# Optimization experiments

Hardware: AMD Instinct MI355X
Metric: run time of the kernel (lower is better)

Reference implementation:

```python
import jax, jax.numpy as jnp
import numpy as np

B, T, F, H = 256, 128, 128, 512

def setup_inputs() -> dict:
    key = jax.random.key(0)
    ks = jax.random.split(key, 20)
    def xavier(k, shape):
        fan_in, fan_out = shape[1], shape[0]
        lim = np.sqrt(6.0 / (fan_in + fan_out)).astype(np.float32)
        return jax.random.uniform(k, shape, jnp.float32, -lim, lim)
    inp = {
        "x": jax.random.normal(ks[0], (B, T, F), jnp.float32),
        "m": (jax.random.uniform(ks[1], (B, T, F)) < 0.8).astype(jnp.float32),
        "d": jax.random.uniform(ks[2], (B, T, F), jnp.float32),
        "target_x": jax.random.normal(ks[3], (B, T, F), jnp.float32),
        "target_mask": (jax.random.uniform(ks[4], (B, T, F)) < 0.2).astype(jnp.float32),
        # TemporalDecay h: W [H,F], b [H]
        "td_h_W": xavier(ks[5], (H, F)), "td_h_b": jnp.zeros((H,), jnp.float32),
        # TemporalDecay x (diag): W [F,F], b [F]
        "td_x_W": xavier(ks[6], (F, F)), "td_x_b": jnp.zeros((F,), jnp.float32),
        # hist_reg Linear(H->F)
        "hist_W": xavier(ks[7], (F, H)), "hist_b": jnp.zeros((F,), jnp.float32),
        "feat_W": xavier(ks[8], (F, F)), "feat_b": jnp.zeros((F,), jnp.float32),
        # weight_combine Linear(2F->F)
        "wc_W": xavier(ks[9], (F, 2 * F)), "wc_b": jnp.zeros((F,), jnp.float32),
        # LSTMCell(2F -> H), PyTorch gate order i,f,g,o
        "W_ih": xavier(ks[10], (4 * H, 2 * F)), "W_hh": xavier(ks[11], (4 * H, H)),
        "b_ih": jnp.zeros((4 * H,), jnp.float32), "b_hh": jnp.zeros((4 * H,), jnp.float32),
    }
    return inp

def _rits_forward(x, m, d, target_x, target_mask,
                  td_h_W, td_h_b, td_x_W, td_x_b,
                  hist_W, hist_b, feat_W, feat_b, wc_W, wc_b,
                  W_ih, W_hh, b_ih, b_hh):
    Bx, Tx, Fx = x.shape
    Hx = td_h_W.shape[0]
    feat_mask = (1.0 - jnp.eye(Fx, dtype=x.dtype))
    feat_Wm_T = (feat_W * feat_mask).T              # [F,F]
    td_x_diag = jnp.diagonal(td_x_W)                # diag mask reduces matmul to elementwise

    def step(carry, inp):
        h, c, loss = carry
        x_t, m_t, d_t, tgt_t, ev_t = inp
        gamma_h = jnp.exp(-jax.nn.relu(d_t @ td_h_W.T + td_h_b))    # [B,H]
        gamma_x = jnp.exp(-jax.nn.relu(d_t * td_x_diag + td_x_b))   # [B,F]
        h = h * gamma_h
        x_hist = h @ hist_W.T + hist_b                              # [B,F]
        x_c = m_t * x_t + (1.0 - m_t) * x_hist
        z_h = x_c @ feat_Wm_T + feat_b
        alpha = jax.nn.sigmoid(jnp.concatenate([gamma_x, m_t], axis=1) @ wc_W.T + wc_b)
        c_h = alpha * z_h + (1.0 - alpha) * x_hist
        c_c = m_t * x_t + (1.0 - m_t) * c_h
        inputs = jnp.concatenate([c_c, m_t], axis=1)                # [B,2F]
        gates = inputs @ W_ih.T + b_ih + h @ W_hh.T + b_hh          # [B,4H]
        i_g, f_g, g_g, o_g = jnp.split(gates, 4, axis=1)
        c = jax.nn.sigmoid(f_g) * c + jax.nn.sigmoid(i_g) * jnp.tanh(g_g)
        h = jax.nn.sigmoid(o_g) * jnp.tanh(c)
        denom = ev_t.sum() + 1e-8
        loss = loss + (((x_hist - tgt_t) ** 2 * ev_t).sum()
                       + ((z_h - tgt_t) ** 2 * ev_t).sum()
                       + ((c_h - tgt_t) ** 2 * ev_t).sum()) / denom
        return (h, c, loss), c_c

    h0 = jnp.zeros((Bx, Hx), x.dtype)
    c0 = jnp.zeros((Bx, Hx), x.dtype)
    tm = lambda a: jnp.swapaxes(a, 0, 1)  # time-major [T,B,F]
    (_, _, loss), imps = jax.lax.scan(
        step, (h0, c0, jnp.float32(0.0)),
        (tm(x), tm(m), tm(d), tm(target_x), tm(target_mask)))
    imputations = jnp.swapaxes(imps, 0, 1)  # [B,T,F]
    return imputations, loss / max(Tx, 1)

def reference(x, m, d, target_x, target_mask,
              td_h_W, td_h_b, td_x_W, td_x_b,
              hist_W, hist_b, feat_W, feat_b, wc_W, wc_b,
              W_ih, W_hh, b_ih, b_hh):
    return _rits_forward(x, m, d, target_x, target_mask,
                         td_h_W, td_h_b, td_x_W, td_x_b,
                         hist_W, hist_b, feat_W, feat_b, wc_W, wc_b,
                         W_ih, W_hh, b_ih, b_hh)
```

## Files before the change

kernel.cpp:

```cpp
#include <hip/hip_runtime.h>

#define DEVINL __device__ __forceinline__

namespace {
constexpr int B = 256, T = 128, F = 128, H = 512;
constexpr int NBLK = 256;
constexpr int NTHR = 1024;

constexpr size_t OFF_NUM    = 0;
constexpr size_t OFF_DEN    = 128;
constexpr size_t OFF_WQCC   = 256;
constexpr size_t OFF_WQH    = OFF_WQCC + 64 * 2048;
constexpr size_t OFF_FSCC   = OFF_WQH + 128 * 2048;
constexpr size_t OFF_FSCHG  = OFF_FSCC + 2048;
constexpr size_t OFF_HISTQ  = OFF_FSCHG + 2048;
constexpr size_t OFF_FSCH   = OFF_HISTQ + 128 * 128;
constexpr size_t OFF_TD2    = OFF_FSCH + 128;
constexpr size_t OFF_FEAT2  = OFF_TD2 + 64 * 512;
constexpr size_t OFF_WC2    = OFF_FEAT2 + 64 * 128;
constexpr size_t OFF_BSUM   = OFF_WC2 + 128 * 128;
constexpr size_t OFF_FDIAG  = OFF_BSUM + 2048;
constexpr size_t WS_WORDS   = OFF_FDIAG + 128;

constexpr float ACT_S  = 15.875f;
constexpr float DEQ_CC = 1.f / (127.f * 15.875f);
constexpr float DEQ_H  = 1.f / (127.f * 127.f);
}

typedef _Float16 h2_t __attribute__((ext_vector_type(2)));

DEVINL h2_t as_h2(unsigned u) { union { unsigned u; h2_t h; } c; c.u = u; return c.h; }
DEVINL unsigned pack2(float a, float b) {
  union { h2_t h; unsigned u; } c;
  c.h = h2_t{(_Float16)a, (_Float16)b};
  return c.u;
}

#if defined(__has_builtin)
#if __has_builtin(__builtin_amdgcn_fdot2)
#define HAVE_FDOT2 1
#endif
#if __has_builtin(__builtin_amdgcn_sdot4)
#define HAVE_SDOT4 1
#endif
#endif
#ifdef HAVE_FDOT2
DEVINL float fdot2(h2_t a, h2_t b, float c) { return __builtin_amdgcn_fdot2(a, b, c, false); }
#else
DEVINL float fdot2(h2_t a, h2_t b, float c) {
  return fmaf((float)a.x, (float)b.x, fmaf((float)a.y, (float)b.y, c));
}
#endif
#ifdef HAVE_SDOT4
DEVINL int sdot4(int a, int b, int c) { return __builtin_amdgcn_sdot4(a, b, c, false); }
#else
DEVINL int sdot4(int a, int b, int c) {
  return c + ((a << 24) >> 24) * ((b << 24) >> 24)
           + ((a << 16) >> 24) * ((b << 16) >> 24)
           + ((a << 8) >> 24) * ((b << 8) >> 24)
           + (a >> 24) * (b >> 24);
}
#endif

DEVINL float fast_sig(float x)  { return 1.f / (1.f + __expf(-x)); }
DEVINL float fast_tanh(float x) { return 1.f - 2.f / (1.f + __expf(2.f * x)); }

DEVINL float wave_sum(float v) {
#pragma unroll
  for (int s = 32; s; s >>= 1) v += __shfl_down(v, s, 64);
  return v;
}
DEVINL float wave_max(float v) {
#pragma unroll
  for (int s = 32; s; s >>= 1) v = fmaxf(v, __shfl_down(v, s, 64));
  return v;
}

__global__ void prep_f16(const float* __restrict__ td_h_W, const float* __restrict__ feat_W,
                         const float* __restrict__ wc_W, const float* __restrict__ b_ih,
                         const float* __restrict__ b_hh,
                         unsigned* __restrict__ wsu, float* __restrict__ wsf) {
  int idx = blockIdx.x * blockDim.x + threadIdx.x;
  if (idx < 32768) {
    const int k2 = idx >> 9, j = idx & 511;
    wsu[OFF_TD2 + idx] = pack2(td_h_W[j * 128 + 2 * k2], td_h_W[j * 128 + 2 * k2 + 1]);
  } else if (idx < 40960) {
    const int i = idx - 32768, k2 = i >> 7, f = i & 127;
    wsu[OFF_FEAT2 + i] = pack2(feat_W[f * 128 + 2 * k2], feat_W[f * 128 + 2 * k2 + 1]);
  } else if (idx < 57344) {
    const int i = idx - 40960, k2 = i >> 7, f = i & 127;
    wsu[OFF_WC2 + i] = pack2(wc_W[f * 256 + 2 * k2], wc_W[f * 256 + 2 * k2 + 1]);
  } else if (idx < 59392) {
    const int i = idx - 57344, unit = i >> 2, g = i & 3;
    wsf[OFF_BSUM + i] = b_ih[g * 512 + unit] + b_hh[g * 512 + unit];
  } else if (idx < 59520) {
    const int f = idx - 59392;
    wsf[OFF_FDIAG + f] = (float)(_Float16)feat_W[f * 129];
  }
}

__global__ void prep_quant_wih(const float* __restrict__ Wih,
                               unsigned* __restrict__ wq, float* __restrict__ fscc) {
  const int col = blockIdx.x;
  const int unit = col >> 2, g = col & 3;
  const float* src = Wih + (size_t)(g * 512 + unit) * 256;
  const int t = threadIdx.x;
  const float4 v = ((const float4*)src)[t];
  float mx = fmaxf(fmaxf(fabsf(v.x), fabsf(v.y)), fmaxf(fabsf(v.z), fabsf(v.w)));
  mx = wave_max(mx);
  mx = __shfl(mx, 0, 64);
  const float s = (mx > 0.f) ? 127.f / mx : 0.f;
  const int q0 = __float2int_rn(v.x * s), q1 = __float2int_rn(v.y * s);
  const int q2 = __float2int_rn(v.z * s), q3 = __float2int_rn(v.w * s);
  wq[t * 2048 + col] =
      (q0 & 0xFF) | ((q1 & 0xFF) << 8) | ((q2 & 0xFF) << 16) | ((q3 & 0xFF) << 24);
  if (t == 0) fscc[col] = mx * DEQ_CC;
}

__global__ void prep_quant_whh(const float* __restrict__ Whh,
                               unsigned* __restrict__ wq, float* __restrict__ fschg) {
  const int col = blockIdx.x;
  const int unit = col >> 2, g = col & 3;
  const float* src = Whh + (size_t)(g * 512 + unit) * 512;
  const int t = threadIdx.x;
  const float4 v = ((const float4*)src)[t];
  float mx = fmaxf(fmaxf(fabsf(v.x), fabsf(v.y)), fmaxf(fabsf(v.z), fabsf(v.w)));
  mx = wave_max(mx);
  __shared__ float wm[2];
  if ((t & 63) == 0) wm[t >> 6] = mx;
  __syncthreads();
  const float maxv = fmaxf(wm[0], wm[1]);
  const float s = (maxv > 0.f) ? 127.f / maxv : 0.f;
  const int q0 = __float2int_rn(v.x * s), q1 = __float2int_rn(v.y * s);
  const int q2 = __float2int_rn(v.z * s), q3 = __float2int_rn(v.w * s);
  wq[t * 2048 + col] =
      (q0 & 0xFF) | ((q1 & 0xFF) << 8) | ((q2 & 0xFF) << 16) | ((q3 & 0xFF) << 24);
  if (t == 0) fschg[col] = maxv * DEQ_H;
}

__global__ void prep_quant_hist(const float* __restrict__ histW,
                                unsigned* __restrict__ histq, float* __restrict__ fsch) {
  const int f = blockIdx.x;
  const float* src = histW + (size_t)f * 512;
  const int t = threadIdx.x;
  const float4 v = ((const float4*)src)[t];
  float mx = fmaxf(fmaxf(fabsf(v.x), fabsf(v.y)), fmaxf(fabsf(v.z), fabsf(v.w)));
  mx = wave_max(mx);
  __shared__ float wm[2];
  if ((t & 63) == 0) wm[t >> 6] = mx;
  __syncthreads();
  const float maxv = fmaxf(wm[0], wm[1]);
  const float s = (maxv > 0.f) ? 127.f / maxv : 0.f;
  const int q0 = __float2int_rn(v.x * s), q1 = __float2int_rn(v.y * s);
  const int q2 = __float2int_rn(v.z * s), q3 = __float2int_rn(v.w * s);
  histq[t * 128 + f] =
      (q0 & 0xFF) | ((q1 & 0xFF) << 8) | ((q2 & 0xFF) << 16) | ((q3 & 0xFF) << 24);
  if (t == 0) fsch[f] = maxv * DEQ_H;
}

__global__ void __launch_bounds__(1024) rits_batch(
    const float* __restrict__ x, const float* __restrict__ m, const float* __restrict__ d,
    const float* __restrict__ tx, const float* __restrict__ tmask,
    const float* __restrict__ td_h_b, const float* __restrict__ td_x_W,
    const float* __restrict__ td_x_b, const float* __restrict__ hist_b,
    const float* __restrict__ feat_b, const float* __restrict__ wc_b,
    const unsigned* __restrict__ wsu, const float* __restrict__ wsf,
    float* __restrict__ num, float* __restrict__ den, float* __restrict__ out)
{
  const int tid = threadIdx.x;
  const int row = blockIdx.x;
  const int unit = tid & 511;
  const int kh = tid >> 9;

  __shared__ unsigned actq[64];
  __shared__ int hq[128];
  __shared__ unsigned d2[64];
  __shared__ unsigned xc2[64];
  __shared__ unsigned gxm2[128];
  __shared__ float xrow[128], mrow[128], drow[128], txrow[128], evrow[128];
  __shared__ int   partI[1024];
  __shared__ float partZ[1024], partA[1024];
  __shared__ int4  partHc[512], partHh[512];
  __shared__ float redA[2], redB[2];

  const float4 bs    = *(const float4*)(wsf + OFF_BSUM + 4 * unit);
  const float4 fscc4 = *(const float4*)(wsf + OFF_FSCC + 4 * unit);
  const float4 fsch4 = *(const float4*)(wsf + OFF_FSCHG + 4 * unit);
  const float tdb = td_h_b[unit];
  const int fc = tid & 127;
  const float hb = hist_b[fc], fb = feat_b[fc], wb = wc_b[fc];
  const float fd = wsf[OFF_FDIAG + fc];
  const float dxw = td_x_W[fc * 129], dxb = td_x_b[fc];
  const float fsch_f = wsf[OFF_FSCH + fc];

  float h0 = 0.f, c0 = 0.f;

  for (int t = 0; t < T; ++t) {
    const int base = (row * T + t) * F;
    float xh_r = 0.f, xc_r = 0.f;

    if (tid < 640) {
      const int a = tid >> 7, f = tid & 127;
      const float v = (a == 0 ? x[base + f] : a == 1 ? m[base + f] : a == 2 ? d[base + f]
                       : a == 3 ? tx[base + f] : tmask[base + f]);
      if      (a == 0) xrow[f]  = v;
      else if (a == 1) mrow[f]  = v;
      else if (a == 2) drow[f]  = v;
      else if (a == 3) txrow[f] = v;
      else             evrow[f] = v;
    } else if (tid < 704) {
      const int k2 = tid - 640;
      d2[k2] = pack2(d[base + 2 * k2], d[base + 2 * k2 + 1]);
    } else if (tid < 768) {
      const int q = tid - 704;
      gxm2[64 + q] = pack2(m[base + 2 * q], m[base + 2 * q + 1]);
    } else if (tid < 800) {
      const int w = tid - 768;
      const int b4 = base + 4 * w;
      const int q0 = __float2int_rn(m[b4] * ACT_S);
      const int q1 = __float2int_rn(m[b4 + 1] * ACT_S);
      const int q2 = __float2int_rn(m[b4 + 2] * ACT_S);
      const int q3 = __float2int_rn(m[b4 + 3] * ACT_S);
      actq[32 + w] =
          (q0 & 0xFF) | ((q1 & 0xFF) << 8) | ((q2 & 0xFF) << 16) | ((q3 & 0xFF) << 24);
    }
    __syncthreads();

    if (tid < 512) {
      float g0 = tdb;
#pragma unroll 8
      for (int k2 = 0; k2 < 64; ++k2)
        g0 = fdot2(as_h2(wsu[OFF_TD2 + (k2 << 9) + tid]), as_h2(d2[k2]), g0);
      h0 *= __expf(-fmaxf(g0, 0.f));
      int q = __float2int_rn(h0 * 127.f);
      const int a1 = __shfl_down(q, 1, 64), a2 = __shfl_down(q, 2, 64), a3 = __shfl_down(q, 3, 64);
      if ((tid & 3) == 0)
        hq[tid >> 2] =
            (q & 0xFF) | ((a1 & 0xFF) << 8) | ((a2 & 0xFF) << 16) | ((a3 & 0xFF) << 24);
    }
    __syncthreads();

    {
      const int kq = tid >> 7;
      int isum = 0;
#pragma unroll 8
      for (int k = 0; k < 16; ++k) {
        const int k4 = kq * 16 + k;
        isum = sdot4((int)wsu[OFF_HISTQ + (k4 << 7) + fc], hq[k4], isum);
      }
      partI[tid] = isum;
    }
    __syncthreads();

    if (tid < 128) {
      int isum = 0;
#pragma unroll
      for (int i = 0; i < 8; ++i) isum += partI[tid + 128 * i];
      xh_r = fmaf((float)isum, fsch_f, hb);
      const float gx = __expf(-fmaxf(fmaf(drow[tid], dxw, dxb), 0.f));
      const float mv = mrow[tid];
      xc_r = mv * xrow[tid] + (1.f - mv) * xh_r;
      const float xcs = __shfl_down(xc_r, 1, 64);
      const float gxs = __shfl_down(gx, 1, 64);
      if (!(tid & 1)) {
        xc2[tid >> 1]  = pack2(xc_r, xcs);
        gxm2[tid >> 1] = pack2(gx, gxs);
      }
    }
    __syncthreads();

    {
      const int kq = tid >> 7;
      float zs = 0.f;
#pragma unroll 8
      for (int k = 0; k < 8; ++k) {
        const int k2 = kq * 8 + k;
        zs = fdot2(as_h2(wsu[OFF_FEAT2 + (k2 << 7) + fc]), as_h2(xc2[k2]), zs);
      }
      partZ[tid] = zs;
      float as = 0.f;
#pragma unroll 8
      for (int k = 0; k < 16; ++k) {
        const int k2 = kq * 16 + k;
        as = fdot2(as_h2(wsu[OFF_WC2 + (k2 << 7) + fc]), as_h2(gxm2[k2]), as);
      }
      partA[tid] = as;
    }
    __syncthreads();

    if (tid < 128) {
      float z = fb, aa = wb;
#pragma unroll
      for (int i = 0; i < 8; ++i) { z += partZ[tid + 128 * i]; aa += partA[tid + 128 * i]; }
      z -= xc_r * fd;
      const float al = fast_sig(aa);
      const float ch = al * z + (1.f - al) * xh_r;
      const float mv = mrow[tid];
      const float cc = mv * xrow[tid] + (1.f - mv) * ch;
      out[base + tid] = cc;
      const float ev = evrow[tid], tg = txrow[tid];
      const float e1 = xh_r - tg, e2 = z - tg, e3 = ch - tg;
      const float s1 = wave_sum(ev * (e1 * e1 + e2 * e2 + e3 * e3));
      const float s2 = wave_sum(ev);
      if ((tid & 63) == 0) { redA[tid >> 6] = s1; redB[tid >> 6] = s2; }
      int qc = __float2int_rn(fminf(fmaxf(cc, -8.f), 8.f) * ACT_S);
      const int c1s = __shfl_down(qc, 1, 64), c2s = __shfl_down(qc, 2, 64), c3s = __shfl_down(qc, 3, 64);
      if (!(tid & 3))
        actq[tid >> 2] =
            (qc & 0xFF) | ((c1s & 0xFF) << 8) | ((c2s & 0xFF) << 16) | ((c3s & 0xFF) << 24);
    }
    __syncthreads();

    {
      if (tid == 1023) {
        atomicAdd(&num[t], redA[0] + redA[1]);
        atomicAdd(&den[t], redB[0] + redB[1]);
      }
      int ci = 0, cf = 0, cg = 0, co = 0;
      const unsigned* wq = wsu + OFF_WQCC + 4 * unit;
#pragma unroll 8
      for (int k = 0; k < 32; ++k) {
        const int k4 = kh * 32 + k;
        const uint4 w = *(const uint4*)(wq + (k4 << 11));
        const int a0 = (int)actq[k4];
        ci = sdot4((int)w.x, a0, ci); cf = sdot4((int)w.y, a0, cf);
        cg = sdot4((int)w.z, a0, cg); co = sdot4((int)w.w, a0, co);
      }
      int hi = 0, hf = 0, hg = 0, ho = 0;
      const unsigned* wh = wsu + OFF_WQH + 4 * unit;
#pragma unroll 8
      for (int k = 0; k < 64; ++k) {
        const int k4 = kh * 64 + k;
        const uint4 w = *(const uint4*)(wh + (k4 << 11));
        const int a0 = hq[k4];
        hi = sdot4((int)w.x, a0, hi); hf = sdot4((int)w.y, a0, hf);
        hg = sdot4((int)w.z, a0, hg); ho = sdot4((int)w.w, a0, ho);
      }
      if (tid >= 512) {
        partHc[unit] = int4{ci, cf, cg, co};
        partHh[unit] = int4{hi, hf, hg, ho};
      }
      __syncthreads();
      if (tid < 512) {
        const int4 pc = partHc[unit], ph = partHh[unit];
        const float ai = bs.x + fscc4.x * (float)(ci + pc.x) + fsch4.x * (float)(hi + ph.x);
        const float af = bs.y + fscc4.y * (float)(cf + pc.y) + fsch4.y * (float)(hf + ph.y);
        const float ag = bs.z + fscc4.z * (float)(cg + pc.z) + fsch4.z * (float)(hg + ph.z);
        const float ao = bs.w + fscc4.w * (float)(co + pc.w) + fsch4.w * (float)(ho + ph.w);
        const float ig = fast_sig(ai), fg = fast_sig(af);
        const float gg = fast_tanh(ag), og = fast_sig(ao);
        c0 = fg * c0 + ig * gg;
        h0 = og * fast_tanh(c0);
      }
    }
    __syncthreads();
  }
}

__global__ void finalize(const float* __restrict__ num, const float* __restrict__ den,
                         float* __restrict__ out) {
  __shared__ float red[2];
  const int t = threadIdx.x;
  float v = num[t] / (den[t] + 1e-8f);
  v = wave_sum(v);
  if ((t & 63) == 0) red[t >> 6] = v;
  __syncthreads();
  if (t == 0) out[(size_t)B * T * F] = (red[0] + red[1]) / (float)T;
}

extern "C" void kernel_launch(void* const* d_in, const int* in_sizes, int n_in,
                              void* d_out, int out_size, void* d_ws, size_t ws_size,
                              hipStream_t stream) {
  const float* x      = (const float*)d_in[0];
  const float* m      = (const float*)d_in[1];
  const float* d      = (const float*)d_in[2];
  const float* tx     = (const float*)d_in[3];
  const float* tmask  = (const float*)d_in[4];
  const float* td_h_W = (const float*)d_in[5];
  const float* td_h_b = (const float*)d_in[6];
  const float* td_x_W = (const float*)d_in[7];
  const float* td_x_b = (const float*)d_in[8];
  const float* hist_W = (const float*)d_in[9];
  const float* hist_b = (const float*)d_in[10];
  const float* feat_W = (const float*)d_in[11];
  const float* feat_b = (const float*)d_in[12];
  const float* wc_W   = (const float*)d_in[13];
  const float* wc_b   = (const float*)d_in[14];
  const float* W_ih   = (const float*)d_in[15];
  const float* W_hh   = (const float*)d_in[16];
  const float* b_ih   = (const float*)d_in[17];
  const float* b_hh   = (const float*)d_in[18];

  float*    wsf = (float*)d_ws;
  unsigned* wsu = (unsigned*)d_ws;
  float*    out = (float*)d_out;

  if (ws_size < WS_WORDS * 4) return;

  hipMemsetAsync(d_ws, 0, 256 * sizeof(float), stream);
  prep_f16<<<dim3((59520 + 255) / 256), dim3(256), 0, stream>>>(
      td_h_W, feat_W, wc_W, b_ih, b_hh, wsu, wsf);
  prep_quant_wih<<<dim3(2048), dim3(64), 0, stream>>>(
      W_ih, wsu + OFF_WQCC, wsf + OFF_FSCC);
  prep_quant_whh<<<dim3(2048), dim3(128), 0, stream>>>(
      W_hh, wsu + OFF_WQH, wsf + OFF_FSCHG);
  prep_quant_hist<<<dim3(128), dim3(128), 0, stream>>>(
      hist_W, wsu + OFF_HISTQ, wsf + OFF_FSCH);
  rits_batch<<<dim3(NBLK), dim3(NTHR), 0, stream>>>(
      x, m, d, tx, tmask, td_h_b, td_x_W, td_x_b, hist_b, feat_b, wc_b,
      wsu, wsf, wsf + OFF_NUM, wsf + OFF_DEN, out);
  finalize<<<dim3(1), dim3(128), 0, stream>>>(wsf + OFF_NUM, wsf + OFF_DEN, out);
}
```

Before: 2.436 ms.

## Cache part of recurrent W_hh int8 weights in registers and LDS

Preloads the first 10 k-slices of the quantized W_hh per thread into registers and the next 7 slices per half into shared memory once before the time loop. Each step then reads only the remaining slices from global or L2, cutting per-step weight traffic in the recurrent matvec. The last timestep also skips the unused LSTM update via an early break. The cost is higher register pressure at 1024 threads per block and about 112KB of extra LDS, which could cause spills or fail to fit.

Result: slower. 3.988 ms (+63.7%).

```diff
diff --git a/kernel.cpp b/kernel.cpp
--- a/kernel.cpp
+++ b/kernel.cpp
@@ -25,6 +25,9 @@
 constexpr float ACT_S  = 15.875f;
 constexpr float DEQ_CC = 1.f / (127.f * 15.875f);
 constexpr float DEQ_H  = 1.f / (127.f * 127.f);
+
+constexpr int NREG = 10;
+constexpr int NLDS = 7;
 }
 
 typedef _Float16 h2_t __attribute__((ext_vector_type(2)));
@@ -34,6 +37,9 @@
   union { h2_t h; unsigned u; } c;
   c.h = h2_t{(_Float16)a, (_Float16)b};
   return c.u;
+}
+DEVINL unsigned pack4i(int a, int b, int c, int d) {
+  return (a & 0xFF) | ((b & 0xFF) << 8) | ((c & 0xFF) << 16) | ((d & 0xFF) << 24);
 }
 
 #if defined(__has_builtin)
@@ -110,10 +116,8 @@
   mx = wave_max(mx);
   mx = __shfl(mx, 0, 64);
   const float s = (mx > 0.f) ? 127.f / mx : 0.f;
-  const int q0 = __float2int_rn(v.x * s), q1 = __float2int_rn(v.y * s);
-  const int q2 = __float2int_rn(v.z * s), q3 = __float2int_rn(v.w * s);
-  wq[t * 2048 + col] =
-      (q0 & 0xFF) | ((q1 & 0xFF) << 8) | ((q2 & 0xFF) << 16) | ((q3 & 0xFF) << 24);
+  wq[t * 2048 + col] = pack4i(__float2int_rn(v.x * s), __float2int_rn(v.y * s),
+                              __float2int_rn(v.z * s), __float2int_rn(v.w * s));
   if (t == 0) fscc[col] = mx * DEQ_CC;
 }
 
@@ -131,10 +135,8 @@
   __syncthreads();
   const float maxv = fmaxf(wm[0], wm[1]);
   const float s = (maxv > 0.f) ? 127.f / maxv : 0.f;
-  const int q0 = __float2int_rn(v.x * s), q1 = __float2int_rn(v.y * s);
-  const int q2 = __float2int_rn(v.z * s), q3 = __float2int_rn(v.w * s);
-  wq[t * 2048 + col] =
-      (q0 & 0xFF) | ((q1 & 0xFF) << 8) | ((q2 & 0xFF) << 16) | ((q3 & 0xFF) << 24);
+  wq[t * 2048 + col] = pack4i(__float2int_rn(v.x * s), __float2int_rn(v.y * s),
+                              __float2int_rn(v.z * s), __float2int_rn(v.w * s));
   if (t == 0) fschg[col] = maxv * DEQ_H;
 }
 
@@ -151,10 +153,8 @@
   __syncthreads();
   const float maxv = fmaxf(wm[0], wm[1]);
   const float s = (maxv > 0.f) ? 127.f / maxv : 0.f;
-  const int q0 = __float2int_rn(v.x * s), q1 = __float2int_rn(v.y * s);
-  const int q2 = __float2int_rn(v.z * s), q3 = __float2int_rn(v.w * s);
-  histq[t * 128 + f] =
-      (q0 & 0xFF) | ((q1 & 0xFF) << 8) | ((q2 & 0xFF) << 16) | ((q3 & 0xFF) << 24);
+  histq[t * 128 + f] = pack4i(__float2int_rn(v.x * s), __float2int_rn(v.y * s),
+                              __float2int_rn(v.z * s), __float2int_rn(v.w * s));
   if (t == 0) fsch[f] = maxv * DEQ_H;
 }
 
@@ -182,6 +182,7 @@
   __shared__ float partZ[1024], partA[1024];
   __shared__ int4  partHc[512], partHh[512];
   __shared__ float redA[2], redB[2];
+  __shared__ __align__(16) unsigned ldsw[2 * NLDS * 2048];
 
   const float4 bs    = *(const float4*)(wsf + OFF_BSUM + 4 * unit);
   const float4 fscc4 = *(const float4*)(wsf + OFF_FSCC + 4 * unit);
@@ -193,7 +194,24 @@
   const float dxw = td_x_W[fc * 129], dxb = td_x_b[fc];
   const float fsch_f = wsf[OFF_FSCH + fc];
 
+  uint4 whr[NREG];
+#pragma unroll
+  for (int j = 0; j < NREG; ++j)
+    whr[j] = *(const uint4*)(wsu + OFF_WQH + ((size_t)(kh * 64 + j) << 11) + 4 * unit);
+#pragma unroll
+  for (int i = 0; i < 2 * NLDS; ++i) {
+    const int q = tid + 1024 * i;
+    const int s = q >> 9;
+    const int o4 = (q & 511) << 2;
+    const int k4 = (s < NLDS) ? (NREG + s) : (64 + NREG + (s - NLDS));
+    if (q < 2 * NLDS * 512)
+      *(uint4*)(ldsw + ((size_t)s << 11) + o4) =
+          *(const uint4*)(wsu + OFF_WQH + ((size_t)k4 << 11) + o4);
+  }
+  const int khs = kh * NLDS;
+
   float h0 = 0.f, c0 = 0.f;
+  __syncthreads();
 
   for (int t = 0; t < T; ++t) {
     const int base = (row * T + t) * F;
@@ -217,12 +235,8 @@
     } else if (tid < 800) {
       const int w = tid - 768;
       const int b4 = base + 4 * w;
-      const int q0 = __float2int_rn(m[b4] * ACT_S);
-      const int q1 = __float2int_rn(m[b4 + 1] * ACT_S);
-      const int q2 = __float2int_rn(m[b4 + 2] * ACT_S);
-      const int q3 = __float2int_rn(m[b4 + 3] * ACT_S);
-      actq[32 + w] =
-          (q0 & 0xFF) | ((q1 & 0xFF) << 8) | ((q2 & 0xFF) << 16) | ((q3 & 0xFF) << 24);
+      actq[32 + w] = pack4i(__float2int_rn(m[b4] * ACT_S), __float2int_rn(m[b4 + 1] * ACT_S),
+                            __float2int_rn(m[b4 + 2] * ACT_S), __float2int_rn(m[b4 + 3] * ACT_S));
     }
     __syncthreads();
 
@@ -235,8 +249,7 @@
       int q = __float2int_rn(h0 * 127.f);
       const int a1 = __shfl_down(q, 1, 64), a2 = __shfl_down(q, 2, 64), a3 = __shfl_down(q, 3, 64);
       if ((tid & 3) == 0)
-        hq[tid >> 2] =
-            (q & 0xFF) | ((a1 & 0xFF) << 8) | ((a2 & 0xFF) << 16) | ((a3 & 0xFF) << 24);
+        hq[tid >> 2] = pack4i(q, a1, a2, a3);
     }
     __syncthreads();
 
@@ -305,17 +318,17 @@
       if ((tid & 63) == 0) { redA[tid >> 6] = s1; redB[tid >> 6] = s2; }
       int qc = __float2int_rn(fminf(fmaxf(cc, -8.f), 8.f) * ACT_S);
       const int c1s = __shfl_down(qc, 1, 64), c2s = __shfl_down(qc, 2, 64), c3s = __shfl_down(qc, 3, 64);
-      if (!(tid & 3))
-        actq[tid >> 2] =
-            (qc & 0xFF) | ((c1s & 0xFF) << 8) | ((c2s & 0xFF) << 16) | ((c3s & 0xFF) << 24);
-    }
-    __syncthreads();
+      if (!(tid & 3)) actq[tid >> 2] = pack4i(qc, c1s, c2s, c3s);
+    }
+    __syncthreads();
+
+    if (tid == 1023) {
+      atomicAdd(&num[t], redA[0] + redA[1]);
+      atomicAdd(&den[t], redB[0] + redB[1]);
+    }
+    if (t == T - 1) break;
 
     {
-      if (tid == 1023) {
-        atomicAdd(&num[t], redA[0] + redA[1]);
-        atomicAdd(&den[t], redB[0] + redB[1]);
-      }
       int ci = 0, cf = 0, cg = 0, co = 0;
       const unsigned* wq = wsu + OFF_WQCC + 4 * unit;
 #pragma unroll 8
@@ -327,11 +340,25 @@
         cg = sdot4((int)w.z, a0, cg); co = sdot4((int)w.w, a0, co);
       }
       int hi = 0, hf = 0, hg = 0, ho = 0;
+#pragma unroll
+      for (int j = 0; j < NREG; ++j) {
+        const int a0 = hq[kh * 64 + j];
+        const uint4 w = whr[j];
+        hi = sdot4((int)w.x, a0, hi); hf = sdot4((int)w.y, a0, hf);
+        hg = sdot4((int)w.z, a0, hg); ho = sdot4((int)w.w, a0, ho);
+      }
+#pragma unroll
+      for (int j = NREG; j < NREG + NLDS; ++j) {
+        const int a0 = hq[kh * 64 + j];
+        const uint4 w = *(const uint4*)(ldsw + ((size_t)(khs + j - NREG) << 11) + 4 * unit);
+        hi = sdot4((int)w.x, a0, hi); hf = sdot4((int)w.y, a0, hf);
+        hg = sdot4((int)w.z, a0, hg); ho = sdot4((int)w.w, a0, ho);
+      }
       const unsigned* wh = wsu + OFF_WQH + 4 * unit;
 #pragma unroll 8
-      for (int k = 0; k < 64; ++k) {
-        const int k4 = kh * 64 + k;
-        const uint4 w = *(const uint4*)(wh + (k4 << 11));
+      for (int j = NREG + NLDS; j < 64; ++j) {
+        const int k4 = kh * 64 + j;
+        const uint4 w = *(const uint4*)(wh + ((size_t)k4 << 11));
         const int a0 = hq[k4];
         hi = sdot4((int)w.x, a0, hi); hf = sdot4((int)w.y, a0, hf);
         hg = sdot4((int)w.z, a0, hg); ho = sdot4((int)w.w, a0, ho);
```
